# Performance work log

Hardware: AMD Instinct MI355X
Metric: run time of the kernel (lower is better)

The kernel has to match this reference:

```python
import jax, jax.numpy as jnp
import numpy as np

B, T, EMB = 2, 2048, 2048
NH, NKV, HD, VHD = 16, 4, 128, 128
N_REP = NH // NKV
ROPE_DIM, ROPE_THETA = 64, 10000.0
WIN = 1024
MLPD = 8192
CS = 2048  # cache size == T: single prefill fills the cache
K_MASK = jnp.finfo(jnp.bfloat16).min
SCALING = HD ** -0.5


def _rope_sincos(positions, rope_dim, theta):
    fraction = jnp.arange(0, rope_dim, 2, dtype=jnp.float32) / rope_dim
    inv_freq = 1.0 / (theta ** fraction)
    ang = jnp.einsum('BT,k->BTk', positions.astype(jnp.float32), inv_freq,
                     precision=jax.lax.Precision.HIGHEST)
    sin, cos = jnp.sin(ang), jnp.cos(ang)
    return jnp.concatenate([sin, sin], -1), jnp.concatenate([cos, cos], -1)


def _rotate_half(x):
    h = x.shape[-1] // 2
    return jnp.concatenate([-x[..., h:], x[..., :h]], -1)


def _apply_rope_partial(x, sin, cos, rope_dim):
    x_rope, x_nope = x[..., :rope_dim], x[..., rope_dim:]
    s, c = sin[:, :, None, :], cos[:, :, None, :]
    x_rope = x_rope * c + _rotate_half(x_rope) * s
    return jnp.concatenate([x_rope, x_nope], -1).astype(x.dtype)


def _rms_norm(x, scale, eps=1e-6):
    xf = x.astype(jnp.float32)
    var = jnp.mean(jnp.square(xf), axis=-1, keepdims=True)
    return (xf * jax.lax.rsqrt(var + eps) * (1.0 + scale)).astype(x.dtype)


def _repeat_kv(h, n_rep):
    if n_rep == 1:
        return h
    b, s, k, d = h.shape
    return jnp.repeat(h[:, :, :, None, :], n_rep, axis=3).reshape(b, s, k * n_rep, d)


def setup_inputs() -> dict:
    key = jax.random.key(0)
    ks = jax.random.split(key, 12)
    s = 0.02
    return {
        'x': jax.random.normal(ks[0], (B, T, EMB), jnp.float32),
        'segment_ids': jnp.ones((B, T), jnp.int32),
        'wq': jax.random.normal(ks[1], (EMB, NH, HD), jnp.float32) * s,
        'wk': jax.random.normal(ks[2], (EMB, NKV, HD), jnp.float32) * s,
        'wv': jax.random.normal(ks[3], (EMB, NKV, VHD), jnp.float32) * s,
        'wo': jax.random.normal(ks[4], (NH, VHD, EMB), jnp.float32) * s,
        'sink_bias': jax.random.normal(ks[5], (NH,), jnp.float32) * s,
        'gate_w': jax.random.normal(ks[6], (EMB, MLPD), jnp.float32) * s,
        'up_w': jax.random.normal(ks[7], (EMB, MLPD), jnp.float32) * s,
        'down_w': jax.random.normal(ks[8], (MLPD, EMB), jnp.float32) * s,
        'norm1_scale': jax.random.normal(ks[9], (EMB,), jnp.float32) * s,
        'norm2_scale': jax.random.normal(ks[10], (EMB,), jnp.float32) * s,
        'k_cache': jnp.zeros((B, CS, NKV, HD), jnp.float32),
        'v_cache': jnp.zeros((B, CS, NKV, VHD), jnp.float32),
    }


def reference(x, segment_ids, wq, wk, wv, wo, sink_bias, gate_w, up_w, down_w,
              norm1_scale, norm2_scale, k_cache, v_cache):
    b, t, _ = x.shape
    cs = k_cache.shape[1]
    cur_ind = jnp.zeros((), jnp.int32)  # fresh cache (prefill)

    # --- attention branch (pre-norm) ---
    h = _rms_norm(x, norm1_scale)
    q = jnp.einsum('BTD,DNH->BTNH', h, wq)
    k = jnp.einsum('BSD,DKH->BSKH', h, wk)
    v = jnp.einsum('BSD,DKV->BSKV', h, wv)

    left_pads = jnp.sum(jnp.cumsum(segment_ids != 0, axis=-1) == 0, -1).astype(jnp.int32)
    start_ind = left_pads  # start_ind initialized to -1 -> set to left_pads
    ar = jnp.arange(t, dtype=jnp.int32)
    first = jnp.argmax(segment_ids, axis=1).astype(jnp.int32)
    positions = jnp.where(segment_ids != 0, ar[None, :] - first[:, None], 2 ** 30) + cur_ind

    sin, cos = _rope_sincos(positions, ROPE_DIM, ROPE_THETA)
    q = _apply_rope_partial(q, sin, cos, ROPE_DIM)
    k = _apply_rope_partial(k, sin, cos, ROPE_DIM)

    k_cache = jax.lax.dynamic_update_slice(k_cache, k, (0, cur_ind, 0, 0))
    v_cache = jax.lax.dynamic_update_slice(v_cache, v, (0, cur_ind, 0, 0))

    kc = _repeat_kv(k_cache, N_REP)  # [B,S,N,H]
    vc = _repeat_kv(v_cache, N_REP)  # [B,S,N,V]

    attn_logits = jnp.einsum('BTNH,BSNH->BTNS', q, kc) * SCALING

    q_pos = cur_ind + ar[None, :] - start_ind[:, None]                      # [B,T]
    ts = jnp.arange(cs, dtype=jnp.int32)
    kv_segment_ids = (ts[None, :] >= start_ind[:, None]) & (ts[None, :] < cur_ind + t)
    k_pos = ts[None, :] - start_ind[:, None]                                # [B,S]
    causal_mask = k_pos[:, None, :] <= q_pos[:, :, None]
    segment_mask = kv_segment_ids[:, None, :] == segment_ids[:, :, None]
    window_mask = k_pos[:, None, :] >= q_pos[:, :, None] - (WIN - 1)
    final_mask = causal_mask & segment_mask & window_mask                    # [B,T,S]

    attn_logits = jnp.where(final_mask[:, :, None, :], attn_logits, K_MASK)

    # learned sink bias: extra logit column, dropped after softmax
    sink = jnp.broadcast_to(sink_bias[None, None, :, None], (b, t, NH, 1))
    attn_logits = jnp.concatenate([attn_logits, sink], axis=-1)
    attn_weights = jax.nn.softmax(attn_logits.astype(jnp.float32), axis=-1).astype(attn_logits.dtype)
    attn_weights = attn_weights[..., :-1]

    attn_out = jnp.einsum('BTNS,BSNV->BTNV', attn_weights, vc)
    attn_out = jnp.einsum('BTNV,NVD->BTD', attn_out, wo)

    x = x + attn_out

    # --- MLP branch (pre-norm, SwiGLU) ---
    h = _rms_norm(x, norm2_scale)
    mlp_out = (jax.nn.silu(h @ gate_w) * (h @ up_w)) @ down_w
    return x + mlp_out
```

## Files before the change

### kernel.cpp

```cpp
#include <hip/hip_runtime.h>
#include <hip/hip_bf16.h>
#include <stdint.h>

#define B_    2
#define T_    2048
#define EMB_  2048
#define NH_   16
#define NKV_  4
#define HD_   128
#define MLPD_ 8192
#define WIN_  1024
#define BT_   (B_ * T_)
#define QKVN_ 3072

typedef __bf16 bf16;
typedef __bf16 bf16x8 __attribute__((ext_vector_type(8)));
typedef float  f32x4  __attribute__((ext_vector_type(4)));

__device__ __forceinline__ bf16 f2b(float f) {
  __hip_bfloat16 h = __float2bfloat16(f);
  return *reinterpret_cast<bf16*>(&h);
}
__device__ __forceinline__ float b2f(bf16 b) {
  __hip_bfloat16 h = *reinterpret_cast<__hip_bfloat16*>(&b);
  return __bfloat162float(h);
}

__device__ __forceinline__ void load_lds16(const void* g, void* l) {
  __builtin_amdgcn_global_load_lds(
      (const __attribute__((address_space(1))) void*)g,
      (__attribute__((address_space(3))) void*)l, 16, 0, 0);
}

__global__ __launch_bounds__(256) void transpose_kernel(
    const float* __restrict__ in, bf16* __restrict__ out, int R, int C,
    int rmul, int radd)
{
  __shared__ float tile[32][33];
  const int tx = threadIdx.x, ty = threadIdx.y;
  const int c0 = blockIdx.x * 32, r0 = blockIdx.y * 32;
  #pragma unroll
  for (int i = 0; i < 32; i += 8)
    tile[ty + i][tx] = in[(long)(r0 + ty + i) * C + c0 + tx];
  __syncthreads();
  #pragma unroll
  for (int i = 0; i < 32; i += 8) {
    const int oc = c0 + ty + i;
    const int orow = (oc & 15) + (((oc >> 4) * rmul + radd) << 4);
    out[(long)orow * R + r0 + tx] = f2b(tile[tx][ty + i]);
  }
}

__global__ __launch_bounds__(256) void rmsnorm_kernel(
    const float* __restrict__ x, const float* __restrict__ scale,
    bf16* __restrict__ out)
{
  const long row = blockIdx.x;
  const float* xr = x + row * EMB_;
  bf16* orow = out + row * EMB_;
  const float4 v0 = ((const float4*)xr)[threadIdx.x];
  const float4 v1 = ((const float4*)xr)[threadIdx.x + 256];
  float ss = v0.x*v0.x + v0.y*v0.y + v0.z*v0.z + v0.w*v0.w
           + v1.x*v1.x + v1.y*v1.y + v1.z*v1.z + v1.w*v1.w;
  #pragma unroll
  for (int off = 32; off >= 1; off >>= 1) ss += __shfl_xor(ss, off, 64);
  __shared__ float red[4];
  if ((threadIdx.x & 63) == 0) red[threadIdx.x >> 6] = ss;
  __syncthreads();
  const float tot = red[0] + red[1] + red[2] + red[3];
  const float rs = rsqrtf(tot * (1.0f / EMB_) + 1e-6f);
  const float4 s0 = ((const float4*)scale)[threadIdx.x];
  const float4 s1 = ((const float4*)scale)[threadIdx.x + 256];
  const int c0 = threadIdx.x * 4;
  orow[c0 + 0]    = f2b(v0.x * rs * (1.0f + s0.x));
  orow[c0 + 1]    = f2b(v0.y * rs * (1.0f + s0.y));
  orow[c0 + 2]    = f2b(v0.z * rs * (1.0f + s0.z));
  orow[c0 + 3]    = f2b(v0.w * rs * (1.0f + s0.w));
  orow[c0 + 1024] = f2b(v1.x * rs * (1.0f + s1.x));
  orow[c0 + 1025] = f2b(v1.y * rs * (1.0f + s1.y));
  orow[c0 + 1026] = f2b(v1.z * rs * (1.0f + s1.z));
  orow[c0 + 1027] = f2b(v1.w * rs * (1.0f + s1.w));
}

template <int EPI>
__global__ __launch_bounds__(256) void gemm_kernel(
    const bf16* __restrict__ A, const bf16* __restrict__ Bt,
    void* __restrict__ out, const float* __restrict__ res,
    int M, int N, int K)
{
  __shared__ __align__(16) bf16 As[128 * 32];
  __shared__ __align__(16) bf16 Bs[128 * 32];
  const int tid  = threadIdx.x;
  const int wave = tid >> 6, lane = tid & 63;
  const int bm = blockIdx.y << 7, bn = blockIdx.x << 7;
  const int wm = (wave & 1) << 6, wn = (wave >> 1) << 6;
  const int l16 = lane & 15, quad = lane >> 4;
  const int srow = lane >> 2, scol = (lane & 3) << 3;

  const bf16* Ap = A  + (long)(bm + wave * 32 + srow) * K + scol;
  const bf16* Bp = Bt + (long)(bn + wave * 32 + srow) * K + scol;
  char* ldsA = (char*)As + wave * 2048;
  char* ldsB = (char*)Bs + wave * 2048;

  f32x4 acc[4][4] = {};

  for (int k0 = 0; k0 < K; k0 += 32) {
    __syncthreads();
    #pragma unroll
    for (int j = 0; j < 2; ++j) {
      load_lds16(Ap + (long)j * 16 * K + k0, ldsA + j * 1024);
      load_lds16(Bp + (long)j * 16 * K + k0, ldsB + j * 1024);
    }
    __syncthreads();
    bf16x8 af[4], bfr[4];
    #pragma unroll
    for (int i = 0; i < 4; ++i) {
      af[i]  = *(const bf16x8*)&As[(wm + i * 16 + l16) * 32 + quad * 8];
      bfr[i] = *(const bf16x8*)&Bs[(wn + i * 16 + l16) * 32 + quad * 8];
    }
    #pragma unroll
    for (int mb = 0; mb < 4; ++mb)
      #pragma unroll
      for (int nb = 0; nb < 4; ++nb)
        acc[mb][nb] = __builtin_amdgcn_mfma_f32_16x16x32_bf16(af[mb], bfr[nb], acc[mb][nb], 0, 0, 0);
  }

  const int crow = bm + wm + (quad << 2);
  const int ccol = bn + wn + l16;
  #pragma unroll
  for (int mb = 0; mb < 4; ++mb)
    #pragma unroll
    for (int nb = 0; nb < 4; ++nb)
      #pragma unroll
      for (int r = 0; r < 4; ++r) {
        const long idx = (long)(crow + mb * 16 + r) * N + (ccol + nb * 16);
        const float v = acc[mb][nb][r];
        if (EPI == 0) {
          ((bf16*)out)[idx] = f2b(v);
        } else {
          ((float*)out)[idx] = v + res[idx];
        }
      }
}

#define GU_BAR()  do { asm volatile("" ::: "memory"); \
                       __builtin_amdgcn_s_barrier(); \
                       asm volatile("" ::: "memory"); } while (0)
#define GU_LGK0() do { asm volatile("s_waitcnt lgkmcnt(0)" ::: "memory"); \
                       __builtin_amdgcn_sched_barrier(0); } while (0)
#define GU_VMC0() asm volatile("s_waitcnt vmcnt(0)" ::: "memory")

#define GU_STAGE(TILE, BB) do { \
    _Pragma("unroll") \
    for (int j_ = 0; j_ < 8; ++j_) \
      load_lds16(srcp[j_] + (long)(TILE) * 64, smem + (BB) + dstoff[j_]); \
  } while (0)

#define GU_READA(BB, MH) do { \
    const char* ab_ = smem + (BB) + wroff; \
    _Pragma("unroll") \
    for (int mb_ = 0; mb_ < 4; ++mb_) { \
      const int rb_ = ((MH) * 64 + mb_ * 16 + l16) * 128; \
      afr[mb_][0] = *(const bf16x8*)(ab_ + rb_ + koff0); \
      afr[mb_][1] = *(const bf16x8*)(ab_ + rb_ + koff1); \
    } } while (0)

#define GU_READB(BB, NH) do { \
    const char* bb_ = smem + (BB) + 32768 + bhoff; \
    _Pragma("unroll") \
    for (int nb_ = 0; nb_ < 2; ++nb_) { \
      const int rb_ = (brow0 + (NH) * 32 + nb_ * 16) * 128; \
      bfr[NH][nb_][0] = *(const bf16x8*)(bb_ + rb_ + koff0); \
      bfr[NH][nb_][1] = *(const bf16x8*)(bb_ + rb_ + koff1); \
    } } while (0)

#define GU_MFMAQ(MH, NH) do { \
    _Pragma("unroll") \
    for (int mb_ = 0; mb_ < 4; ++mb_) \
      _Pragma("unroll") \
      for (int nb_ = 0; nb_ < 2; ++nb_) { \
        f32x4* a_ = &acc[(MH) * 4 + mb_][(NH) * 2 + nb_]; \
        *a_ = __builtin_amdgcn_mfma_f32_16x16x32_bf16(afr[mb_][0], bfr[NH][nb_][0], *a_, 0, 0, 0); \
        *a_ = __builtin_amdgcn_mfma_f32_16x16x32_bf16(afr[mb_][1], bfr[NH][nb_][1], *a_, 0, 0, 0); \
      } } while (0)

__global__ __launch_bounds__(512, 2) void mlp_gateup256_kernel(
    const bf16* __restrict__ A, const bf16* __restrict__ Bc,
    bf16* __restrict__ out, int M, int Ncat, int K)
{
  (void)M;
  __shared__ __align__(16) char smem[131072];
  const int tid  = threadIdx.x;
  const int wave = tid >> 6, lane = tid & 63;
  const int quad = lane >> 4, l16 = lane & 15;
  const int wr = wave >> 2, wc = wave & 3;
  const int bm = blockIdx.y << 8, bn = blockIdx.x << 8;
  const int KT = K >> 6;

  const int koff0 = (quad * 16) ^ ((l16 & 7) << 4);
  const int koff1 = koff0 ^ 64;
  const int wroff = wr * 16384;
  const int bhoff = (wc >> 1) * 16384;
  const int brow0 = (wc & 1) * 64 + l16;

  const int srow = lane >> 3;
  const int scol = ((lane & 7) ^ srow) << 3;
  const bf16* srcp[8]; int dstoff[8];
  #pragma unroll
  for (int op = 0; op < 2; ++op)
    #pragma unroll
    for (int h = 0; h < 2; ++h)
      #pragma unroll
      for (int g = 0; g < 2; ++g) {
        const int j = op * 4 + h * 2 + g;
        const int grow = (op ? bn : bm) + h * 128 + g * 64 + wave * 8 + srow;
        srcp[j] = (op ? Bc : A) + (long)grow * K + scol;
        dstoff[j] = op * 32768 + h * 16384 + g * 8192 + wave * 1024;
      }

  f32x4 acc[8][4] = {};
  bf16x8 afr[4][2];
  bf16x8 bfr[2][2][2];

  GU_STAGE(0, 0);
  GU_VMC0();
  GU_BAR();

  #pragma unroll 1
  for (int t = 0; t < KT; t += 2) {
    GU_STAGE(t + 1, 65536);
    GU_READA(0, 0); GU_READB(0, 0);
    GU_BAR(); GU_LGK0();
    __builtin_amdgcn_s_setprio(1); GU_MFMAQ(0, 0); __builtin_amdgcn_s_setprio(0);
    GU_BAR();
    GU_READB(0, 1);
    GU_BAR(); GU_LGK0();
    __builtin_amdgcn_s_setprio(1); GU_MFMAQ(0, 1); __builtin_amdgcn_s_setprio(0);
    GU_BAR();
    GU_READA(0, 1);
    GU_BAR(); GU_LGK0();
    __builtin_amdgcn_s_setprio(1); GU_MFMAQ(1, 1); __builtin_amdgcn_s_setprio(0);
    GU_BAR();
    __builtin_amdgcn_s_setprio(1); GU_MFMAQ(1, 0); __builtin_amdgcn_s_setprio(0);
    GU_VMC0();
    GU_BAR();
    if (t + 2 < KT) GU_STAGE(t + 2, 0);
    GU_READA(65536, 0); GU_READB(65536, 0);
    GU_BAR(); GU_LGK0();
    __builtin_amdgcn_s_setprio(1); GU_MFMAQ(0, 0); __builtin_amdgcn_s_setprio(0);
    GU_BAR();
    GU_READB(65536, 1);
    GU_BAR(); GU_LGK0();
    __builtin_amdgcn_s_setprio(1); GU_MFMAQ(0, 1); __builtin_amdgcn_s_setprio(0);
    GU_BAR();
    GU_READA(65536, 1);
    GU_BAR(); GU_LGK0();
    __builtin_amdgcn_s_setprio(1); GU_MFMAQ(1, 1); __builtin_amdgcn_s_setprio(0);
    GU_BAR();
    __builtin_amdgcn_s_setprio(1); GU_MFMAQ(1, 0); __builtin_amdgcn_s_setprio(0);
    GU_VMC0();
    GU_BAR();
  }

  const long NO = Ncat >> 1;
  const int orow0 = bm + wr * 128 + (quad << 2);
  const int ocol  = (bn >> 1) + wc * 32 + l16;
  #pragma unroll
  for (int ma = 0; ma < 8; ++ma)
    #pragma unroll
    for (int nh = 0; nh < 2; ++nh)
      #pragma unroll
      for (int r = 0; r < 4; ++r) {
        const float g = acc[ma][nh * 2][r];
        const float u = acc[ma][nh * 2 + 1][r];
        out[(long)(orow0 + ma * 16 + r) * NO + ocol + nh * 16] =
            f2b(g / (1.0f + __expf(-g)) * u);
      }
}

__global__ __launch_bounds__(512) void down_kernel(
    const bf16* __restrict__ A, const bf16* __restrict__ Bt,
    float* __restrict__ out, const float* __restrict__ res,
    int M, int N, int K)
{
  __shared__ __align__(16) char smem[24576];
  const int tid = threadIdx.x;
  const int wave = tid >> 6, lane = tid & 63;
  const int role = wave >> 2, wq = wave & 3;
  const int wm = (wq & 1) << 6, wn = (wq >> 1) << 6;
  const int l16 = lane & 15, quad = lane >> 4;
  const int srow = lane >> 2, scol = (lane & 3) << 3;

  const int bm = blockIdx.y << 8, bn = blockIdx.x << 7;

  const bf16* sp[3]; char* dp[3];
  #pragma unroll
  for (int j = 0; j < 3; ++j) {
    const int c = 3 * wave + j;
    const int buf = c >> 3, r0 = (c & 7) << 4;
    const bf16* gbase = (buf == 0) ? A + (long)bm * K
                      : (buf == 1) ? A + (long)(bm + 128) * K
                                   : Bt + (long)bn * K;
    sp[j] = gbase + (long)(r0 + srow) * K + scol;
    dp[j] = smem + buf * 8192 + (c & 7) * 1024;
  }
  const bf16* Asb = (const bf16*)(smem + role * 8192);
  const bf16* Bsb = (const bf16*)(smem + 16384);

  f32x4 acc[4][4] = {};

  for (int k0 = 0; k0 < K; k0 += 32) {
    __syncthreads();
    #pragma unroll
    for (int j = 0; j < 3; ++j) load_lds16(sp[j] + k0, dp[j]);
    __syncthreads();
    bf16x8 af[4], bfr[4];
    #pragma unroll
    for (int i = 0; i < 4; ++i) {
      af[i]  = *(const bf16x8*)&Asb[(wm + i * 16 + l16) * 32 + quad * 8];
      bfr[i] = *(const bf16x8*)&Bsb[(wn + i * 16 + l16) * 32 + quad * 8];
    }
    #pragma unroll
    for (int mb = 0; mb < 4; ++mb)
      #pragma unroll
      for (int nb = 0; nb < 4; ++nb)
        acc[mb][nb] = __builtin_amdgcn_mfma_f32_16x16x32_bf16(af[mb], bfr[nb], acc[mb][nb], 0, 0, 0);
  }

  const int crow = bm + role * 128 + wm + (quad << 2);
  const int ccol = bn + wn + l16;
  #pragma unroll
  for (int mb = 0; mb < 4; ++mb)
    #pragma unroll
    for (int nb = 0; nb < 4; ++nb)
      #pragma unroll
      for (int r = 0; r < 4; ++r) {
        const long idx = (long)(crow + mb * 16 + r) * N + (ccol + nb * 16);
        out[idx] = acc[mb][nb][r] + res[idx];
      }
}

__global__ __launch_bounds__(256) void rope_kernel(
    const bf16* __restrict__ qkv, bf16* __restrict__ Q,
    bf16* __restrict__ K, bf16* __restrict__ VT)
{
  const int t = blockIdx.x, b = blockIdx.y;
  const bf16* row = qkv + (long)(b * T_ + t) * QKVN_;
  const float tf = (float)t;
  for (int idx = threadIdx.x; idx < NH_ * HD_; idx += 256) {
    const int head = idx >> 7, hd = idx & 127;
    const float v = b2f(row[idx]);
    float o;
    if (hd < 64) {
      const int j = hd & 31;
      const float ang = tf * expf(-(float)j * 0.28782313662425574f);
      const float sn = sinf(ang), cs = cosf(ang);
      o = (hd < 32) ? (v * cs - b2f(row[idx + 32]) * sn)
                    : (v * cs + b2f(row[idx - 32]) * sn);
    } else o = v;
    Q[((long)(b * NH_ + head) * T_ + t) * HD_ + hd] = f2b(o);
  }
  for (int idx = threadIdx.x; idx < NKV_ * HD_; idx += 256) {
    const int kv = idx >> 7, hd = idx & 127;
    const float v = b2f(row[NH_ * HD_ + idx]);
    float o;
    if (hd < 64) {
      const int j = hd & 31;
      const float ang = tf * expf(-(float)j * 0.28782313662425574f);
      const float sn = sinf(ang), cs = cosf(ang);
      o = (hd < 32) ? (v * cs - b2f(row[NH_ * HD_ + idx + 32]) * sn)
                    : (v * cs + b2f(row[NH_ * HD_ + idx - 32]) * sn);
    } else o = v;
    K[((long)(b * NKV_ + kv) * T_ + t) * HD_ + hd] = f2b(o);
  }
  for (int idx = threadIdx.x; idx < NKV_ * HD_; idx += 256) {
    const int kv = idx >> 7, vd = idx & 127;
    VT[((long)(b * NKV_ + kv) * HD_ + vd) * T_ + t] = row[(NH_ + NKV_) * HD_ + idx];
  }
}

__global__ __launch_bounds__(256) void attn_kernel(
    const bf16* __restrict__ Q, const bf16* __restrict__ Kg,
    const bf16* __restrict__ VTg, const float* __restrict__ sink,
    bf16* __restrict__ attnb)
{
  __shared__ __align__(16) bf16 Qs[64 * 136];
  __shared__ __align__(16) bf16 Ks[64 * 136];
  __shared__ __align__(16) bf16 Vs[128 * 72];
  __shared__ __align__(16) bf16 Ps[64 * 72];

  const int qt = blockIdx.x;
  const int bh = blockIdx.y;
  const int b = bh >> 4, h = bh & 15;
  const int kvh = h >> 2;
  const int t0 = qt * 64;
  const int tid = threadIdx.x;
  const int wave = tid >> 6, lane = tid & 63;
  const int quad = lane >> 4, l16 = lane & 15;

  const bf16* Qp = Q + ((long)(b * NH_ + h) * T_ + t0) * HD_;
  #pragma unroll
  for (int c = tid; c < 1024; c += 256) {
    const int r = c >> 4, cc = (c & 15) << 3;
    *(uint4*)&Qs[r * 136 + cc] = *(const uint4*)&Qp[r * HD_ + cc];
  }

  float m_i[4], l_i[4];
  const float sb = sink[h];
  #pragma unroll
  for (int r = 0; r < 4; ++r) { m_i[r] = sb; l_i[r] = 1.0f; }
  f32x4 Oacc[8] = {};

  const int st_lo = (qt > 16) ? (qt - 16) : 0;
  for (int st = st_lo; st <= qt; ++st) {
    const int s0 = st * 64;
    __syncthreads();
    const bf16* Kp = Kg + ((long)(b * NKV_ + kvh) * T_ + s0) * HD_;
    #pragma unroll
    for (int c = tid; c < 1024; c += 256) {
      const int r = c >> 4, cc = (c & 15) << 3;
      *(uint4*)&Ks[r * 136 + cc] = *(const uint4*)&Kp[r * HD_ + cc];
    }
    const bf16* Vp = VTg + (long)(b * NKV_ + kvh) * HD_ * T_ + s0;
    #pragma unroll
    for (int c = tid; c < 1024; c += 256) {
      const int r = c >> 3, cc = (c & 7) << 3;
      *(uint4*)&Vs[r * 72 + cc] = *(const uint4*)&Vp[(long)r * T_ + cc];
    }
    __syncthreads();

    f32x4 sacc[4] = {};
    #pragma unroll
    for (int kb = 0; kb < 4; ++kb) {
      const bf16x8 aq = *(const bf16x8*)&Qs[(wave * 16 + l16) * 136 + kb * 32 + quad * 8];
      #pragma unroll
      for (int nb = 0; nb < 4; ++nb) {
        const bf16x8 bk = *(const bf16x8*)&Ks[(nb * 16 + l16) * 136 + kb * 32 + quad * 8];
        sacc[nb] = __builtin_amdgcn_mfma_f32_16x16x32_bf16(aq, bk, sacc[nb], 0, 0, 0);
      }
    }

    float sv[4][4];
    float rmax[4] = {-INFINITY, -INFINITY, -INFINITY, -INFINITY};
    const int colb = s0 + l16;
    const int rowb = t0 + wave * 16 + quad * 4;
    #pragma unroll
    for (int nb = 0; nb < 4; ++nb)
      #pragma unroll
      for (int r = 0; r < 4; ++r) {
        float v = sacc[nb][r] * 0.08838834764831845f;
        const int s = colb + nb * 16, tq = rowb + r;
        if (s > tq || s < tq - (WIN_ - 1)) v = -INFINITY;
        sv[nb][r] = v;
        rmax[r] = fmaxf(rmax[r], v);
      }
    #pragma unroll
    for (int r = 0; r < 4; ++r)
      #pragma unroll
      for (int off = 1; off < 16; off <<= 1)
        rmax[r] = fmaxf(rmax[r], __shfl_xor(rmax[r], off, 64));
    float alpha[4], rsum[4];
    #pragma unroll
    for (int r = 0; r < 4; ++r) {
      const float mn = fmaxf(m_i[r], rmax[r]);
      alpha[r] = __expf(m_i[r] - mn);
      m_i[r] = mn;
      rsum[r] = 0.0f;
    }
    #pragma unroll
    for (int nb = 0; nb < 4; ++nb)
      #pragma unroll
      for (int r = 0; r < 4; ++r) {
        const float p = __expf(sv[nb][r] - m_i[r]);
        rsum[r] += p;
        Ps[(wave * 16 + quad * 4 + r) * 72 + nb * 16 + l16] = f2b(p);
      }
    #pragma unroll
    for (int r = 0; r < 4; ++r) {
      #pragma unroll
      for (int off = 1; off < 16; off <<= 1)
        rsum[r] += __shfl_xor(rsum[r], off, 64);
      l_i[r] = l_i[r] * alpha[r] + rsum[r];
    }
    #pragma unroll
    for (int nb = 0; nb < 8; ++nb)
      #pragma unroll
      for (int r = 0; r < 4; ++r)
        Oacc[nb][r] *= alpha[r];
    __syncthreads();

    #pragma unroll
    for (int ks = 0; ks < 2; ++ks) {
      const bf16x8 ap = *(const bf16x8*)&Ps[(wave * 16 + l16) * 72 + ks * 32 + quad * 8];
      #pragma unroll
      for (int nb = 0; nb < 8; ++nb) {
        const bf16x8 bv = *(const bf16x8*)&Vs[(nb * 16 + l16) * 72 + ks * 32 + quad * 8];
        Oacc[nb] = __builtin_amdgcn_mfma_f32_16x16x32_bf16(ap, bv, Oacc[nb], 0, 0, 0);
      }
    }
  }

  float rcp[4];
  #pragma unroll
  for (int r = 0; r < 4; ++r) rcp[r] = 1.0f / l_i[r];
  bf16* outp = attnb + ((long)(b * T_ + t0 + wave * 16 + quad * 4)) * EMB_ + h * HD_ + l16;
  #pragma unroll
  for (int nb = 0; nb < 8; ++nb)
    #pragma unroll
    for (int r = 0; r < 4; ++r)
      outp[(long)r * EMB_ + nb * 16] = f2b(Oacc[nb][r] * rcp[r]);
}

extern "C" void kernel_launch(void* const* d_in, const int* in_sizes, int n_in,
                              void* d_out, int out_size, void* d_ws, size_t ws_size,
                              hipStream_t stream)
{
  (void)in_sizes; (void)n_in; (void)out_size; (void)ws_size;
  const float* x    = (const float*)d_in[0];
  const float* wq   = (const float*)d_in[2];
  const float* wk   = (const float*)d_in[3];
  const float* wv   = (const float*)d_in[4];
  const float* wo   = (const float*)d_in[5];
  const float* sink = (const float*)d_in[6];
  const float* gw   = (const float*)d_in[7];
  const float* uw   = (const float*)d_in[8];
  const float* dw   = (const float*)d_in[9];
  const float* n1   = (const float*)d_in[10];
  const float* n2   = (const float*)d_in[11];

  char* base = (char*)d_ws;
  bf16*  hbuf  = (bf16*)base;
  char*  R1    = base + (size_t)16777216;
  char*  R2    = R1   + (size_t)67108864;
  bf16*  mact  = (bf16*)(R2 + (size_t)33554432);

  bf16* qkv   = (bf16*)R1;
  bf16* Qb    = (bf16*)(R1 + 25165824);
  bf16* Kb    = (bf16*)(R1 + 41943040);
  bf16* VTb   = (bf16*)(R1 + 46137344);
  bf16* attnb = (bf16*)R1;
  bf16* wqkvT = (bf16*)R2;
  bf16* woT   = (bf16*)(R2 + 12582912);
  bf16* Bcat  = (bf16*)R1;
  bf16* downT = (bf16*)R2;
  float* x1   = (float*)d_out;

  const dim3 tb(32, 8);
  transpose_kernel<<<dim3( 64,  64), tb, 0, stream>>>(wq, wqkvT,                      EMB_, EMB_, 1, 0);
  transpose_kernel<<<dim3( 16,  64), tb, 0, stream>>>(wk, wqkvT + (size_t)2048*EMB_,  EMB_, 512, 1, 0);
  transpose_kernel<<<dim3( 16,  64), tb, 0, stream>>>(wv, wqkvT + (size_t)2560*EMB_,  EMB_, 512, 1, 0);
  transpose_kernel<<<dim3( 64,  64), tb, 0, stream>>>(wo, woT,                        EMB_, EMB_, 1, 0);

  rmsnorm_kernel<<<BT_, 256, 0, stream>>>(x, n1, hbuf);
  gemm_kernel<0><<<dim3(QKVN_/128, BT_/128), 256, 0, stream>>>(hbuf, wqkvT, qkv, nullptr, BT_, QKVN_, EMB_);
  rope_kernel<<<dim3(T_, B_), 256, 0, stream>>>(qkv, Qb, Kb, VTb);
  attn_kernel<<<dim3(T_/64, B_*NH_), 256, 0, stream>>>(Qb, Kb, VTb, sink, attnb);
  gemm_kernel<1><<<dim3(EMB_/128, BT_/128), 256, 0, stream>>>(attnb, woT, x1, x, BT_, EMB_, EMB_);

  rmsnorm_kernel<<<BT_, 256, 0, stream>>>(x1, n2, hbuf);
  transpose_kernel<<<dim3(256,  64), tb, 0, stream>>>(gw, Bcat, EMB_, MLPD_, 2, 0);
  transpose_kernel<<<dim3(256,  64), tb, 0, stream>>>(uw, Bcat, EMB_, MLPD_, 2, 1);
  mlp_gateup256_kernel<<<dim3((2*MLPD_)/256, BT_/256), 512, 0, stream>>>(hbuf, Bcat, mact, BT_, 2*MLPD_, EMB_);
  transpose_kernel<<<dim3( 64, 256), tb, 0, stream>>>(dw, downT, MLPD_, EMB_, 1, 0);
  down_kernel<<<dim3(EMB_/128, BT_/256), 512, 0, stream>>>(mact, downT, (float*)d_out, x1, BT_, EMB_, MLPD_);
}
```

Measured before the change: 1.097 ms.

## Replace QKV, output and down GEMMs with a triple-buffered 128x256 pipelined kernel

Swaps the simple single-buffered 128x128 GEMM and the down-projection kernel for one 512-thread kernel using 128x256 tiles, BK=64, XOR-swizzled LDS layout, and a three-stage global-to-LDS prefetch pipeline. MFMA issue is split into two halves with priority raising and explicit waitcnt and barriers. The intent is to hide memory latency, avoid LDS bank conflicts and raise arithmetic intensity per block. In exchange it uses 144KB of LDS per block, which limits occupancy, and on smaller N (2048) it yields fewer blocks per wave.

```diff
diff --git a/kernel.cpp b/kernel.cpp
--- a/kernel.cpp
+++ b/kernel.cpp
@@ -82,51 +82,103 @@
   orow[c0 + 1027] = f2b(v1.w * rs * (1.0f + s1.w));
 }
 
+#define DG_BAR()  do { asm volatile("" ::: "memory"); \
+                       __builtin_amdgcn_s_barrier(); \
+                       asm volatile("" ::: "memory"); } while (0)
+#define DG_LGK0() do { asm volatile("s_waitcnt lgkmcnt(0)" ::: "memory"); \
+                       __builtin_amdgcn_sched_barrier(0); } while (0)
+
+#define DG_STAGE(TILE, BB) do { \
+    _Pragma("unroll") \
+    for (int j_ = 0; j_ < 6; ++j_) \
+      load_lds16(srcp[j_] + (long)(TILE) * 64, smem + (BB) + dstoff[j_]); \
+  } while (0)
+
+#define DG_READA(BB) do { \
+    _Pragma("unroll") \
+    for (int mb_ = 0; mb_ < 4; ++mb_) { \
+      const int rb_ = (wr * 64 + mb_ * 16 + l16) * 128; \
+      afr[mb_][0] = *(const bf16x8*)(smem + (BB) + rb_ + koff0); \
+      afr[mb_][1] = *(const bf16x8*)(smem + (BB) + rb_ + koff1); \
+    } } while (0)
+
+#define DG_READB(BB, NH) do { \
+    _Pragma("unroll") \
+    for (int nb_ = 0; nb_ < 2; ++nb_) { \
+      const int rb_ = 16384 + (wc * 64 + (NH) * 32 + nb_ * 16 + l16) * 128; \
+      bfr[nb_][0] = *(const bf16x8*)(smem + (BB) + rb_ + koff0); \
+      bfr[nb_][1] = *(const bf16x8*)(smem + (BB) + rb_ + koff1); \
+    } } while (0)
+
+#define DG_MFMA(NH) do { \
+    _Pragma("unroll") \
+    for (int mb_ = 0; mb_ < 4; ++mb_) \
+      _Pragma("unroll") \
+      for (int nb_ = 0; nb_ < 2; ++nb_) { \
+        f32x4* a_ = &acc[mb_][(NH) * 2 + nb_]; \
+        *a_ = __builtin_amdgcn_mfma_f32_16x16x32_bf16(afr[mb_][0], bfr[nb_][0], *a_, 0, 0, 0); \
+        *a_ = __builtin_amdgcn_mfma_f32_16x16x32_bf16(afr[mb_][1], bfr[nb_][1], *a_, 0, 0, 0); \
+      } } while (0)
+
 template <int EPI>
-__global__ __launch_bounds__(256) void gemm_kernel(
+__global__ __launch_bounds__(512, 2) void gemm256_kernel(
     const bf16* __restrict__ A, const bf16* __restrict__ Bt,
     void* __restrict__ out, const float* __restrict__ res,
     int M, int N, int K)
 {
-  __shared__ __align__(16) bf16 As[128 * 32];
-  __shared__ __align__(16) bf16 Bs[128 * 32];
+  (void)M;
+  __shared__ __align__(16) char smem[147456];
   const int tid  = threadIdx.x;
   const int wave = tid >> 6, lane = tid & 63;
-  const int bm = blockIdx.y << 7, bn = blockIdx.x << 7;
-  const int wm = (wave & 1) << 6, wn = (wave >> 1) << 6;
-  const int l16 = lane & 15, quad = lane >> 4;
-  const int srow = lane >> 2, scol = (lane & 3) << 3;
-
-  const bf16* Ap = A  + (long)(bm + wave * 32 + srow) * K + scol;
-  const bf16* Bp = Bt + (long)(bn + wave * 32 + srow) * K + scol;
-  char* ldsA = (char*)As + wave * 2048;
-  char* ldsB = (char*)Bs + wave * 2048;
+  const int quad = lane >> 4, l16 = lane & 15;
+  const int wr = wave >> 2, wc = wave & 3;
+  const int bm = blockIdx.y << 7, bn = blockIdx.x << 8;
+  const int KT = K >> 6;
+
+  const int koff0 = (quad * 16) ^ ((l16 & 7) << 4);
+  const int koff1 = koff0 ^ 64;
+
+  const int srow = lane >> 3;
+  const int scol = ((lane & 7) ^ srow) << 3;
+  const bf16* srcp[6]; int dstoff[6];
+  #pragma unroll
+  for (int j = 0; j < 6; ++j) {
+    const int c = 6 * wave + j;
+    const int grow = (c < 16) ? (bm + c * 8 + srow) : (bn + (c - 16) * 8 + srow);
+    const bf16* gbase = (c < 16) ? A : Bt;
+    srcp[j] = gbase + (long)grow * K + scol;
+    dstoff[j] = c * 1024;
+  }
 
   f32x4 acc[4][4] = {};
-
-  for (int k0 = 0; k0 < K; k0 += 32) {
-    __syncthreads();
-    #pragma unroll
-    for (int j = 0; j < 2; ++j) {
-      load_lds16(Ap + (long)j * 16 * K + k0, ldsA + j * 1024);
-      load_lds16(Bp + (long)j * 16 * K + k0, ldsB + j * 1024);
-    }
-    __syncthreads();
-    bf16x8 af[4], bfr[4];
-    #pragma unroll
-    for (int i = 0; i < 4; ++i) {
-      af[i]  = *(const bf16x8*)&As[(wm + i * 16 + l16) * 32 + quad * 8];
-      bfr[i] = *(const bf16x8*)&Bs[(wn + i * 16 + l16) * 32 + quad * 8];
-    }
-    #pragma unroll
-    for (int mb = 0; mb < 4; ++mb)
-      #pragma unroll
-      for (int nb = 0; nb < 4; ++nb)
-        acc[mb][nb] = __builtin_amdgcn_mfma_f32_16x16x32_bf16(af[mb], bfr[nb], acc[mb][nb], 0, 0, 0);
-  }
-
-  const int crow = bm + wm + (quad << 2);
-  const int ccol = bn + wn + l16;
+  bf16x8 afr[4][2];
+  bf16x8 bfr[2][2];
+
+  int base0 = 0, base1 = 49152, base2 = 98304;
+
+  DG_STAGE(0, base0);
+  DG_STAGE(1, base1);
+  asm volatile("s_waitcnt vmcnt(0)" ::: "memory");
+  DG_BAR();
+
+  #pragma unroll 1
+  for (int t = 0; t < KT; ++t) {
+    if (t + 2 < KT) DG_STAGE(t + 2, base2);
+    DG_READA(base0); DG_READB(base0, 0);
+    DG_BAR(); DG_LGK0();
+    __builtin_amdgcn_s_setprio(1); DG_MFMA(0); __builtin_amdgcn_s_setprio(0);
+    DG_BAR();
+    DG_READB(base0, 1);
+    DG_BAR(); DG_LGK0();
+    __builtin_amdgcn_s_setprio(1); DG_MFMA(1); __builtin_amdgcn_s_setprio(0);
+    if (t + 2 < KT) { asm volatile("s_waitcnt vmcnt(6)" ::: "memory"); }
+    else            { asm volatile("s_waitcnt vmcnt(0)" ::: "memory"); }
+    DG_BAR();
+    const int r_ = base0; base0 = base1; base1 = base2; base2 = r_;
+  }
+
+  const int crow = bm + wr * 64 + (quad << 2);
+  const int ccol = bn + wc * 64 + l16;
   #pragma unroll
   for (int mb = 0; mb < 4; ++mb)
     #pragma unroll
@@ -275,68 +327,6 @@
         const float u = acc[ma][nh * 2 + 1][r];
         out[(long)(orow0 + ma * 16 + r) * NO + ocol + nh * 16] =
             f2b(g / (1.0f + __expf(-g)) * u);
-      }
-}
-
-__global__ __launch_bounds__(512) void down_kernel(
-    const bf16* __restrict__ A, const bf16* __restrict__ Bt,
-    float* __restrict__ out, const float* __restrict__ res,
-    int M, int N, int K)
-{
-  __shared__ __align__(16) char smem[24576];
-  const int tid = threadIdx.x;
-  const int wave = tid >> 6, lane = tid & 63;
-  const int role = wave >> 2, wq = wave & 3;
-  const int wm = (wq & 1) << 6, wn = (wq >> 1) << 6;
-  const int l16 = lane & 15, quad = lane >> 4;
-  const int srow = lane >> 2, scol = (lane & 3) << 3;
-
-  const int bm = blockIdx.y << 8, bn = blockIdx.x << 7;
-
-  const bf16* sp[3]; char* dp[3];
-  #pragma unroll
-  for (int j = 0; j < 3; ++j) {
-    const int c = 3 * wave + j;
-    const int buf = c >> 3, r0 = (c & 7) << 4;
-    const bf16* gbase = (buf == 0) ? A + (long)bm * K
-                      : (buf == 1) ? A + (long)(bm + 128) * K
-                                   : Bt + (long)bn * K;
-    sp[j] = gbase + (long)(r0 + srow) * K + scol;
-    dp[j] = smem + buf * 8192 + (c & 7) * 1024;
-  }
-  const bf16* Asb = (const bf16*)(smem + role * 8192);
-  const bf16* Bsb = (const bf16*)(smem + 16384);
-
-  f32x4 acc[4][4] = {};
-
-  for (int k0 = 0; k0 < K; k0 += 32) {
-    __syncthreads();
-    #pragma unroll
-    for (int j = 0; j < 3; ++j) load_lds16(sp[j] + k0, dp[j]);
-    __syncthreads();
-    bf16x8 af[4], bfr[4];
-    #pragma unroll
-    for (int i = 0; i < 4; ++i) {
-      af[i]  = *(const bf16x8*)&Asb[(wm + i * 16 + l16) * 32 + quad * 8];
-      bfr[i] = *(const bf16x8*)&Bsb[(wn + i * 16 + l16) * 32 + quad * 8];
-    }
-    #pragma unroll
-    for (int mb = 0; mb < 4; ++mb)
-      #pragma unroll
-      for (int nb = 0; nb < 4; ++nb)
-        acc[mb][nb] = __builtin_amdgcn_mfma_f32_16x16x32_bf16(af[mb], bfr[nb], acc[mb][nb], 0, 0, 0);
-  }
-
-  const int crow = bm + role * 128 + wm + (quad << 2);
-  const int ccol = bn + wn + l16;
-  #pragma unroll
-  for (int mb = 0; mb < 4; ++mb)
-    #pragma unroll
-    for (int nb = 0; nb < 4; ++nb)
-      #pragma unroll
-      for (int r = 0; r < 4; ++r) {
-        const long idx = (long)(crow + mb * 16 + r) * N + (ccol + nb * 16);
-        out[idx] = acc[mb][nb][r] + res[idx];
       }
 }
 
@@ -552,15 +542,15 @@
   transpose_kernel<<<dim3( 64,  64), tb, 0, stream>>>(wo, woT,                        EMB_, EMB_, 1, 0);
 
   rmsnorm_kernel<<<BT_, 256, 0, stream>>>(x, n1, hbuf);
-  gemm_kernel<0><<<dim3(QKVN_/128, BT_/128), 256, 0, stream>>>(hbuf, wqkvT, qkv, nullptr, BT_, QKVN_, EMB_);
+  gemm256_kernel<0><<<dim3(QKVN_/256, BT_/128), 512, 0, stream>>>(hbuf, wqkvT, qkv, nullptr, BT_, QKVN_, EMB_);
   rope_kernel<<<dim3(T_, B_), 256, 0, stream>>>(qkv, Qb, Kb, VTb);
   attn_kernel<<<dim3(T_/64, B_*NH_), 256, 0, stream>>>(Qb, Kb, VTb, sink, attnb);
-  gemm_kernel<1><<<dim3(EMB_/128, BT_/128), 256, 0, stream>>>(attnb, woT, x1, x, BT_, EMB_, EMB_);
+  gemm256_kernel<1><<<dim3(EMB_/256, BT_/128), 512, 0, stream>>>(attnb, woT, x1, x, BT_, EMB_, EMB_);
 
   rmsnorm_kernel<<<BT_, 256, 0, stream>>>(x1, n2, hbuf);
   transpose_kernel<<<dim3(256,  64), tb, 0, stream>>>(gw, Bcat, EMB_, MLPD_, 2, 0);
   transpose_kernel<<<dim3(256,  64), tb, 0, stream>>>(uw, Bcat, EMB_, MLPD_, 2, 1);
   mlp_gateup256_kernel<<<dim3((2*MLPD_)/256, BT_/256), 512, 0, stream>>>(hbuf, Bcat, mact, BT_, 2*MLPD_, EMB_);
   transpose_kernel<<<dim3( 64, 256), tb, 0, stream>>>(dw, downT, MLPD_, EMB_, 1, 0);
-  down_kernel<<<dim3(EMB_/128, BT_/256), 512, 0, stream>>>(mact, downT, (float*)d_out, x1, BT_, EMB_, MLPD_);
-}
+  gemm256_kernel<1><<<dim3(EMB_/256, BT_/128), 512, 0, stream>>>(mact, downT, (float*)d_out, x1, BT_, EMB_, MLPD_);
+}
```

Result: faster. 962.3 us (-12.3%).
